# Optimization experiments

Hardware: AMD Instinct MI355X
Metric: run time of the kernel (lower is better)

The kernel has to match this reference:

```python
import jax, jax.numpy as jnp
import numpy as np

B, D, U, R, H, ND = 32768, 1024, 1024, 4, 16, 11


def setup_inputs() -> dict:
    key = jax.random.key(0)
    ks = jax.random.split(key, 12)
    s = 0.02
    return {
        "x": jax.random.normal(ks[0], (B, D), dtype=jnp.float32),
        "domain_indicator": jax.random.randint(ks[1], (B, 1), 0, ND, dtype=jnp.int32),
        "kernel": jax.random.normal(ks[2], (D, U), dtype=jnp.float32) * s,
        "bias": jnp.zeros((U,), dtype=jnp.float32),
        "a_kernel": jax.random.normal(ks[3], (ND, D, R), dtype=jnp.float32) * s,
        "b_kernel": jax.random.normal(ks[4], (ND, R, U), dtype=jnp.float32) * s,
        "domain_bias": jnp.zeros((ND, U), dtype=jnp.float32),
        "WQ": jax.random.normal(ks[5], (R, H), dtype=jnp.float32) * s,
        "WK": jax.random.normal(ks[6], (R, H), dtype=jnp.float32) * s,
        "WV": jax.random.normal(ks[7], (R, H), dtype=jnp.float32) * s,
        "linear": jax.random.normal(ks[8], (H, R), dtype=jnp.float32) * s,
        "factor": jax.random.normal(ks[9], (1, ND), dtype=jnp.float32) * s,
    }


def reference(x, domain_indicator, kernel, bias, a_kernel, b_kernel,
              domain_bias, WQ, WK, WV, linear, factor):
    # Base dense path (dropout inactive at inference)
    out = x @ kernel + bias  # [B, U]

    # Per-domain LoRA-A gather (domains 1..10) and projection: [B, 10, R]
    dA = jnp.einsum('bd,ndr->bnr', x, a_kernel[1:11])

    # Tiny self-attention over the 10 domain projections
    Q = dA @ WQ  # [B, 10, H]
    Kt = dA @ WK
    V = dA @ WV
    scale = 1.0 / jnp.sqrt(jnp.float32(H))
    A = jax.nn.softmax(jnp.einsum('bnh,bmh->bnm', Q, Kt) * scale, axis=-1)
    O = jnp.einsum('bnm,bmh->bnh', A, V) @ linear  # [B, 10, R]

    # Sum over domains -> shared LoRA latent [B, R]
    dom = jnp.sum(O, axis=1)

    # Per-domain LoRA-B expansion: [B, 10, U]
    dB = jnp.einsum('br,nru->bnu', dom, b_kernel[1:11])

    # Domain mixture weights (softmax over all n_domain, cols 1..10 used)
    w = jax.nn.softmax(factor, axis=-1)[0, 1:11]  # [10]
    dout = jnp.einsum('bnu,n->bu', dB, w)  # [B, U]

    # Domain bias from the indicator of the first row
    idx = domain_indicator[0, 0]
    dout = dout + domain_bias[idx]

    return jax.nn.relu(out + dout)
```

## Files before the change

kernel.cpp:

```cpp
#include <hip/hip_runtime.h>
#include <hip/hip_bf16.h>


typedef float f32x4 __attribute__((ext_vector_type(4)));
typedef short s16x8 __attribute__((ext_vector_type(8)));
typedef unsigned int u32x4 __attribute__((ext_vector_type(4)));

#define WS_DOM    0u
#define WS_BEFF   524288u
#define WS_BIAS   540672u
#define WS_G      544768u
#define WS_M      545024u
#define WS_ACATT  545280u
#define WS_KB     679936u
#define WS_XB     2777088u

__device__ __forceinline__ unsigned short f2bf(float f) {
  unsigned int u = __builtin_bit_cast(unsigned int, f);
  u += 0x7fffu + ((u >> 16) & 1u);
  return (unsigned short)(u >> 16);
}
__device__ __forceinline__ unsigned int f2bf2(float a, float b) {
  return (unsigned int)f2bf(a) | ((unsigned int)f2bf(b) << 16);
}

__device__ __forceinline__ void gload_lds16(const void* g, void* l) {
  __builtin_amdgcn_global_load_lds((const __attribute__((address_space(1))) void*)g,
                                   (__attribute__((address_space(3))) void*)l, 16, 0, 0);
}

__global__ void prep1(const float* __restrict__ factor, const float* __restrict__ WQ,
                      const float* __restrict__ WK, const float* __restrict__ WV,
                      const float* __restrict__ linear, const float* __restrict__ bias,
                      const float* __restrict__ domain_bias, const float* __restrict__ b_kernel,
                      const int* __restrict__ dom_ind, float* __restrict__ ws_f) {
  __shared__ float wsm[10];
  const int t = threadIdx.x;
  float* G    = ws_f + (WS_G >> 2);
  float* M    = ws_f + (WS_M >> 2);
  float* beff = ws_f + (WS_BEFF >> 2);
  float* btot = ws_f + (WS_BIAS >> 2);
  if (t == 0) {
    float f[11], mx = -1e30f;
    for (int i = 0; i < 11; i++) { f[i] = factor[i]; mx = fmaxf(mx, f[i]); }
    float s = 0.f;
    for (int i = 0; i < 11; i++) { f[i] = expf(f[i] - mx); s += f[i]; }
    float inv = 1.0f / s;
    for (int i = 0; i < 10; i++) wsm[i] = f[i + 1] * inv;
  }
  if (t < 16) {
    int r = t >> 2, c = t & 3;
    float g = 0.f, m = 0.f;
    for (int h = 0; h < 16; h++) {
      g += WQ[r * 16 + h] * WK[c * 16 + h];
      m += WV[r * 16 + h] * linear[h * 4 + c];
    }
    G[t] = 0.25f * g;
    M[t] = m;
  }
  __syncthreads();
  const int idx = dom_ind[0];
  for (int u = t; u < 1024; u += 256) btot[u] = bias[u] + domain_bias[idx * 1024 + u];
  for (int i = t; i < 4096; i += 256) {
    int r = i >> 10, u = i & 1023;
    float s = 0.f;
    for (int n = 0; n < 10; n++) s += wsm[n] * b_kernel[(1 + n) * 4096 + r * 1024 + u];
    beff[i] = s;
  }
}

__global__ void prep2(const float* __restrict__ a_kernel, unsigned short* __restrict__ acatt) {
  const int i = blockIdx.x * 256 + threadIdx.x;
  const int c = i >> 10, d = i & 1023;
  float v = 0.0f;
  if (c < 40) v = a_kernel[(1 + (c >> 2)) * 4096 + d * 4 + (c & 3)];
  acatt[i] = f2bf(v);
}

__global__ void transK(const float* __restrict__ kern, unsigned short* __restrict__ kb) {
  __shared__ float tile[32][33];
  const int t = threadIdx.x;
  const int kt = blockIdx.x >> 5, nt = blockIdx.x & 31;
  const int k0 = kt << 5, n0 = nt << 5;
  const int row = t >> 5, col = t & 31;
#pragma unroll
  for (int i = 0; i < 4; i++)
    tile[row + i * 8][col] = kern[(k0 + row + i * 8) * 1024 + n0 + col];
  __syncthreads();
  const int nrow = t >> 3, kq = t & 7;
  uint2 pv;
  pv.x = f2bf2(tile[kq * 4 + 0][nrow], tile[kq * 4 + 1][nrow]);
  pv.y = f2bf2(tile[kq * 4 + 2][nrow], tile[kq * 4 + 3][nrow]);
  *reinterpret_cast<uint2*>(&kb[(n0 + nrow) * 1024 + k0 + kq * 4]) = pv;
}

template <bool WRITEXB>
__launch_bounds__(256, 3)
__global__ void stageA(const float* __restrict__ x, const unsigned short* __restrict__ acatt,
                       const float* __restrict__ ws_f, float* __restrict__ dom,
                       unsigned short* __restrict__ xb) {
  __shared__ unsigned short As[16 * 1024];
  __shared__ float dAs[4][16][49];
  const int t = threadIdx.x;
  const int rows0 = blockIdx.x << 4;

  f32x4 v[16];
#pragma unroll
  for (int j = 0; j < 16; j++)
    v[j] = *reinterpret_cast<const f32x4*>(x + (size_t)(rows0 + j) * 1024 + (t << 2));
#pragma unroll
  for (int j = 0; j < 16; j++) {
    uint2 p;
    p.x = f2bf2(v[j][0], v[j][1]);
    p.y = f2bf2(v[j][2], v[j][3]);
    if (WRITEXB)
      *reinterpret_cast<uint2*>(xb + (size_t)(rows0 + j) * 1024 + (t << 2)) = p;
    *reinterpret_cast<uint2*>(As + (((j << 10) + (t << 2)) ^ ((j & 7) << 3))) = p;
  }
  __syncthreads();

  const int w = t >> 6, l = t & 63;
  const int lr = l & 15, kg = l >> 4;
  const f32x4 zero4 = {0.f, 0.f, 0.f, 0.f};
  f32x4 acc[3]; acc[0] = zero4; acc[1] = zero4; acc[2] = zero4;
#pragma unroll
  for (int s = 0; s < 8; s++) {
    const int kelem = (w << 8) + (s << 5) + (kg << 3);
    s16x8 av = *reinterpret_cast<const s16x8*>(As + (((lr << 10) + kelem) ^ ((lr & 7) << 3)));
#pragma unroll
    for (int nf = 0; nf < 3; nf++) {
      s16x8 bv = *reinterpret_cast<const s16x8*>(acatt + ((nf << 4) + lr) * 1024 + kelem);
      acc[nf] = __builtin_amdgcn_mfma_f32_16x16x32_bf16(av, bv, acc[nf], 0, 0, 0);
    }
  }
#pragma unroll
  for (int nf = 0; nf < 3; nf++) {
    const int col = (nf << 4) + lr;
    if (col < 40) {
#pragma unroll
      for (int j = 0; j < 4; j++)
        dAs[w][(kg << 2) + j][col] = acc[nf][j];
    }
  }
  __syncthreads();

  if (t < 16) {
    const int row = t;
    const float* Gp = ws_f + (WS_G >> 2);
    const float* Mp = ws_f + (WS_M >> 2);
    float dA[10][4];
#pragma unroll
    for (int m = 0; m < 10; m++)
#pragma unroll
      for (int r = 0; r < 4; r++)
        dA[m][r] = dAs[0][row][(m << 2) + r] + dAs[1][row][(m << 2) + r]
                 + dAs[2][row][(m << 2) + r] + dAs[3][row][(m << 2) + r];
    float Gv[16], Mv[16];
#pragma unroll
    for (int i = 0; i < 16; i++) { Gv[i] = Gp[i]; Mv[i] = Mp[i]; }
    float tm[10][4];
#pragma unroll
    for (int m = 0; m < 10; m++)
#pragma unroll
      for (int r = 0; r < 4; r++)
        tm[m][r] = Gv[(r << 2) + 0] * dA[m][0] + Gv[(r << 2) + 1] * dA[m][1]
                 + Gv[(r << 2) + 2] * dA[m][2] + Gv[(r << 2) + 3] * dA[m][3];
    float cm[10];
#pragma unroll
    for (int m = 0; m < 10; m++) cm[m] = 0.f;
#pragma unroll
    for (int n = 0; n < 10; n++) {
      float sv[10]; float mx = -1e30f;
#pragma unroll
      for (int m = 0; m < 10; m++) {
        float s = dA[n][0] * tm[m][0] + dA[n][1] * tm[m][1]
                + dA[n][2] * tm[m][2] + dA[n][3] * tm[m][3];
        sv[m] = s; mx = fmaxf(mx, s);
      }
      float ssum = 0.f;
#pragma unroll
      for (int m = 0; m < 10; m++) { float e = expf(sv[m] - mx); sv[m] = e; ssum += e; }
      float inv = 1.0f / ssum;
#pragma unroll
      for (int m = 0; m < 10; m++) cm[m] += sv[m] * inv;
    }
    float u0 = 0.f, u1 = 0.f, u2 = 0.f, u3 = 0.f;
#pragma unroll
    for (int m = 0; m < 10; m++) {
      u0 += cm[m] * dA[m][0]; u1 += cm[m] * dA[m][1];
      u2 += cm[m] * dA[m][2]; u3 += cm[m] * dA[m][3];
    }
    f32x4 dv;
#pragma unroll
    for (int rp = 0; rp < 4; rp++)
      dv[rp] = u0 * Mv[rp] + u1 * Mv[4 + rp] + u2 * Mv[8 + rp] + u3 * Mv[12 + rp];
    *reinterpret_cast<f32x4*>(&dom[(rows0 + row) << 2]) = dv;
  }
}

template <bool XB>
__launch_bounds__(256, 3)
__global__ void mainGEMM(const float* __restrict__ x, const unsigned short* __restrict__ xb,
                         const unsigned short* __restrict__ kb,
                         const float* __restrict__ ws_f, float* __restrict__ out) {
  __shared__ unsigned short As[8192];
  __shared__ unsigned short Bs[8192];
  const int t = threadIdx.x;
  const int w = t >> 6, l = t & 63;
  const int b = blockIdx.x;
  const int xcd = b & 7, i6 = b >> 3;
  const int bm = (xcd << 5) + (i6 >> 3), bn = i6 & 7;
  const int rows0 = bm << 7, cols0 = bn << 7;
  const int wr = w >> 1, wc = w & 1;
  const int lr = l & 15, kg = l >> 4;
  const float* dom  = ws_f + (WS_DOM >> 2);
  const float* beff = ws_f + (WS_BEFF >> 2);
  const float* btot = ws_f + (WS_BIAS >> 2);
  const f32x4 zero4 = {0.f, 0.f, 0.f, 0.f};
  f32x4 acc[4][4];
#pragma unroll
  for (int i = 0; i < 4; i++)
#pragma unroll
    for (int j = 0; j < 4; j++) acc[i][j] = zero4;

#pragma unroll 1
  for (int kc = 0; kc < 16; kc++) {
    if (kc) __syncthreads();
#pragma unroll
    for (int i = 0; i < 4; i++) {
      int segid = i * 256 + t;
      int c = segid >> 3, ks = segid & 7;
      gload_lds16(kb + (cols0 + c) * 1024 + (kc << 6) + ((ks ^ (c & 7)) << 3), Bs + segid * 8);
    }
#pragma unroll
    for (int i = 0; i < 4; i++) {
      int segid = i * 256 + t;
      int row = segid >> 3, ks = segid & 7;
      if (XB) {
        gload_lds16(xb + (rows0 + row) * 1024 + (kc << 6) + ((ks ^ (row & 7)) << 3),
                    As + segid * 8);
      } else {
        const float* gp = x + (rows0 + row) * 1024 + (kc << 6) + (ks << 3);
        f32x4 v0 = *reinterpret_cast<const f32x4*>(gp);
        f32x4 v1 = *reinterpret_cast<const f32x4*>(gp + 4);
        u32x4 o = { f2bf2(v0[0], v0[1]), f2bf2(v0[2], v0[3]),
                    f2bf2(v1[0], v1[1]), f2bf2(v1[2], v1[3]) };
        *reinterpret_cast<u32x4*>(As + row * 64 + ((ks ^ (row & 7)) << 3)) = o;
      }
    }
    __syncthreads();
#pragma unroll
    for (int kh = 0; kh < 2; kh++) {
      const int cp = (kh << 2) + kg;
      s16x8 av[4], bv[4];
#pragma unroll
      for (int mf = 0; mf < 4; mf++) {
        int arow = (wr << 6) + (mf << 4) + lr;
        av[mf] = *reinterpret_cast<const s16x8*>(As + arow * 64 + ((cp ^ (arow & 7)) << 3));
      }
#pragma unroll
      for (int nf = 0; nf < 4; nf++) {
        int brow = (wc << 6) + (nf << 4) + lr;
        bv[nf] = *reinterpret_cast<const s16x8*>(Bs + brow * 64 + ((cp ^ (brow & 7)) << 3));
      }
#pragma unroll
      for (int mf = 0; mf < 4; mf++)
#pragma unroll
        for (int nf = 0; nf < 4; nf++)
          acc[mf][nf] = __builtin_amdgcn_mfma_f32_16x16x32_bf16(av[mf], bv[nf], acc[mf][nf], 0, 0, 0);
    }
  }

  float bcv[4], bev[4][4];
#pragma unroll
  for (int nf = 0; nf < 4; nf++) {
    int col = cols0 + (wc << 6) + (nf << 4) + lr;
    bcv[nf] = btot[col];
#pragma unroll
    for (int r = 0; r < 4; r++) bev[nf][r] = beff[r * 1024 + col];
  }
#pragma unroll
  for (int mf = 0; mf < 4; mf++) {
    const int rbase = rows0 + (wr << 6) + (mf << 4) + (kg << 2);
    f32x4 dm[4];
#pragma unroll
    for (int j = 0; j < 4; j++)
      dm[j] = *reinterpret_cast<const f32x4*>(dom + ((rbase + j) << 2));
#pragma unroll
    for (int nf = 0; nf < 4; nf++) {
      const int col = cols0 + (wc << 6) + (nf << 4) + lr;
#pragma unroll
      for (int j = 0; j < 4; j++) {
        float v = acc[mf][nf][j] + bcv[nf]
                + dm[j][0] * bev[nf][0] + dm[j][1] * bev[nf][1]
                + dm[j][2] * bev[nf][2] + dm[j][3] * bev[nf][3];
        out[(rbase + j) * 1024 + col] = fmaxf(v, 0.f);
      }
    }
  }
}

extern "C" void kernel_launch(void* const* d_in, const int* in_sizes, int n_in,
                              void* d_out, int out_size, void* d_ws, size_t ws_size,
                              hipStream_t stream) {
  (void)in_sizes; (void)n_in; (void)out_size;
  const float* x           = (const float*)d_in[0];
  const int*   dom_ind     = (const int*)d_in[1];
  const float* kern        = (const float*)d_in[2];
  const float* bias        = (const float*)d_in[3];
  const float* a_kernel    = (const float*)d_in[4];
  const float* b_kernel    = (const float*)d_in[5];
  const float* domain_bias = (const float*)d_in[6];
  const float* WQ          = (const float*)d_in[7];
  const float* WK          = (const float*)d_in[8];
  const float* WV          = (const float*)d_in[9];
  const float* linear      = (const float*)d_in[10];
  const float* factor      = (const float*)d_in[11];
  float* out = (float*)d_out;
  char* ws = (char*)d_ws;
  float* ws_f = (float*)ws;
  unsigned short* acatt = (unsigned short*)(ws + WS_ACATT);
  unsigned short* kb    = (unsigned short*)(ws + WS_KB);
  unsigned short* xb    = (unsigned short*)(ws + WS_XB);
  float* dom            = (float*)(ws + WS_DOM);
  const bool use_xb = ws_size >= (size_t)WS_XB + (size_t)32768 * 1024 * 2;

  prep1<<<1, 256, 0, stream>>>(factor, WQ, WK, WV, linear, bias, domain_bias, b_kernel, dom_ind, ws_f);
  prep2<<<256, 256, 0, stream>>>(a_kernel, acatt);
  transK<<<1024, 256, 0, stream>>>(kern, kb);
  if (use_xb) {
    stageA<true><<<2048, 256, 0, stream>>>(x, acatt, ws_f, dom, xb);
    mainGEMM<true><<<2048, 256, 0, stream>>>(x, xb, kb, ws_f, out);
  } else {
    stageA<false><<<2048, 256, 0, stream>>>(x, acatt, ws_f, dom, xb);
    mainGEMM<false><<<2048, 256, 0, stream>>>(x, xb, kb, ws_f, out);
  }
}
```

Measured before the change: 181.3 us.

## Split fp32-to-bf16 conversion of x into separate kernel before LoRA stage

Moves the x fp32-to-bf16 conversion into a dedicated streaming kernel, convX. The LoRA-A stage then reads the bf16 copy into LDS through direct global-to-LDS loads, with a swizzle applied on the global address, and preloads the acatt B fragments into registers before the barrier. This is meant to separate the bandwidth-bound conversion from the MFMA stage and overlap loads. The cost is an extra kernel launch and an extra read of the bf16 x buffer (64 MB) by stageL.

```diff
diff --git a/kernel.cpp b/kernel.cpp
--- a/kernel.cpp
+++ b/kernel.cpp
@@ -94,16 +94,131 @@
   *reinterpret_cast<uint2*>(&kb[(n0 + nrow) * 1024 + k0 + kq * 4]) = pv;
 }
 
-template <bool WRITEXB>
+__global__ void convX(const float* __restrict__ x, unsigned short* __restrict__ xb) {
+  const size_t i0 = (size_t)blockIdx.x * 256 + threadIdx.x;
+#pragma unroll
+  for (int it = 0; it < 8; ++it) {
+    const size_t u = i0 + (size_t)it * 524288;
+    const float* gp = x + u * 8;
+    f32x4 a = *reinterpret_cast<const f32x4*>(gp);
+    f32x4 b = *reinterpret_cast<const f32x4*>(gp + 4);
+    u32x4 o = { f2bf2(a[0], a[1]), f2bf2(a[2], a[3]),
+                f2bf2(b[0], b[1]), f2bf2(b[2], b[3]) };
+    *reinterpret_cast<u32x4*>(xb + u * 8) = o;
+  }
+}
+
 __launch_bounds__(256, 3)
-__global__ void stageA(const float* __restrict__ x, const unsigned short* __restrict__ acatt,
-                       const float* __restrict__ ws_f, float* __restrict__ dom,
-                       unsigned short* __restrict__ xb) {
+__global__ void stageL(const unsigned short* __restrict__ xb,
+                       const unsigned short* __restrict__ acatt,
+                       const float* __restrict__ ws_f, float* __restrict__ dom) {
   __shared__ unsigned short As[16 * 1024];
   __shared__ float dAs[4][16][49];
   const int t = threadIdx.x;
   const int rows0 = blockIdx.x << 4;
-
+  const int w = t >> 6, l = t & 63;
+  const int lr = l & 15, kg = l >> 4;
+
+#pragma unroll
+  for (int i = 0; i < 8; i++) {
+    const int segid = i * 256 + t;
+    const int row = segid >> 7;
+    const int ks = segid & 127;
+    gload_lds16(xb + (size_t)(rows0 + row) * 1024 + ((ks ^ (row & 7)) << 3),
+                As + segid * 8);
+  }
+  s16x8 bvr[8][3];
+#pragma unroll
+  for (int s = 0; s < 8; s++) {
+    const int kelem = (w << 8) + (s << 5) + (kg << 3);
+#pragma unroll
+    for (int nf = 0; nf < 3; nf++)
+      bvr[s][nf] = *reinterpret_cast<const s16x8*>(acatt + ((nf << 4) + lr) * 1024 + kelem);
+  }
+  __syncthreads();
+
+  const f32x4 zero4 = {0.f, 0.f, 0.f, 0.f};
+  f32x4 acc[3]; acc[0] = zero4; acc[1] = zero4; acc[2] = zero4;
+#pragma unroll
+  for (int s = 0; s < 8; s++) {
+    const int kelem = (w << 8) + (s << 5) + (kg << 3);
+    s16x8 av = *reinterpret_cast<const s16x8*>(As + (((lr << 10) + kelem) ^ ((lr & 7) << 3)));
+#pragma unroll
+    for (int nf = 0; nf < 3; nf++)
+      acc[nf] = __builtin_amdgcn_mfma_f32_16x16x32_bf16(av, bvr[s][nf], acc[nf], 0, 0, 0);
+  }
+#pragma unroll
+  for (int nf = 0; nf < 3; nf++) {
+    const int col = (nf << 4) + lr;
+    if (col < 40) {
+#pragma unroll
+      for (int j = 0; j < 4; j++)
+        dAs[w][(kg << 2) + j][col] = acc[nf][j];
+    }
+  }
+  __syncthreads();
+
+  if (t < 16) {
+    const int row = t;
+    const float* Gp = ws_f + (WS_G >> 2);
+    const float* Mp = ws_f + (WS_M >> 2);
+    float dA[10][4];
+#pragma unroll
+    for (int m = 0; m < 10; m++)
+#pragma unroll
+      for (int r = 0; r < 4; r++)
+        dA[m][r] = dAs[0][row][(m << 2) + r] + dAs[1][row][(m << 2) + r]
+                 + dAs[2][row][(m << 2) + r] + dAs[3][row][(m << 2) + r];
+    float Gv[16], Mv[16];
+#pragma unroll
+    for (int i = 0; i < 16; i++) { Gv[i] = Gp[i]; Mv[i] = Mp[i]; }
+    float tm[10][4];
+#pragma unroll
+    for (int m = 0; m < 10; m++)
+#pragma unroll
+      for (int r = 0; r < 4; r++)
+        tm[m][r] = Gv[(r << 2) + 0] * dA[m][0] + Gv[(r << 2) + 1] * dA[m][1]
+                 + Gv[(r << 2) + 2] * dA[m][2] + Gv[(r << 2) + 3] * dA[m][3];
+    float cm[10];
+#pragma unroll
+    for (int m = 0; m < 10; m++) cm[m] = 0.f;
+#pragma unroll
+    for (int n = 0; n < 10; n++) {
+      float sv[10]; float mx = -1e30f;
+#pragma unroll
+      for (int m = 0; m < 10; m++) {
+        float s = dA[n][0] * tm[m][0] + dA[n][1] * tm[m][1]
+                + dA[n][2] * tm[m][2] + dA[n][3] * tm[m][3];
+        sv[m] = s; mx = fmaxf(mx, s);
+      }
+      float ssum = 0.f;
+#pragma unroll
+      for (int m = 0; m < 10; m++) { float e = expf(sv[m] - mx); sv[m] = e; ssum += e; }
+      float inv = 1.0f / ssum;
+#pragma unroll
+      for (int m = 0; m < 10; m++) cm[m] += sv[m] * inv;
+    }
+    float u0 = 0.f, u1 = 0.f, u2 = 0.f, u3 = 0.f;
+#pragma unroll
+    for (int m = 0; m < 10; m++) {
+      u0 += cm[m] * dA[m][0]; u1 += cm[m] * dA[m][1];
+      u2 += cm[m] * dA[m][2]; u3 += cm[m] * dA[m][3];
+    }
+    f32x4 dv;
+#pragma unroll
+    for (int rp = 0; rp < 4; rp++)
+      dv[rp] = u0 * Mv[rp] + u1 * Mv[4 + rp] + u2 * Mv[8 + rp] + u3 * Mv[12 + rp];
+    *reinterpret_cast<f32x4*>(&dom[(rows0 + row) << 2]) = dv;
+  }
+}
+
+__launch_bounds__(256, 3)
+__global__ void stageA_f32(const float* __restrict__ x, const unsigned short* __restrict__ acatt,
+                           const float* __restrict__ ws_f, float* __restrict__ dom) {
+  __shared__ unsigned short As[16 * 1024];
+  __shared__ float dAs[4][16][49];
+  const int t = threadIdx.x;
+  const int rows0 = blockIdx.x << 4;
   f32x4 v[16];
 #pragma unroll
   for (int j = 0; j < 16; j++)
@@ -113,12 +228,9 @@
     uint2 p;
     p.x = f2bf2(v[j][0], v[j][1]);
     p.y = f2bf2(v[j][2], v[j][3]);
-    if (WRITEXB)
-      *reinterpret_cast<uint2*>(xb + (size_t)(rows0 + j) * 1024 + (t << 2)) = p;
     *reinterpret_cast<uint2*>(As + (((j << 10) + (t << 2)) ^ ((j & 7) << 3))) = p;
   }
   __syncthreads();
-
   const int w = t >> 6, l = t & 63;
   const int lr = l & 15, kg = l >> 4;
   const f32x4 zero4 = {0.f, 0.f, 0.f, 0.f};
@@ -143,7 +255,6 @@
     }
   }
   __syncthreads();
-
   if (t < 16) {
     const int row = t;
     const float* Gp = ws_f + (WS_G >> 2);
@@ -329,10 +440,11 @@
   prep2<<<256, 256, 0, stream>>>(a_kernel, acatt);
   transK<<<1024, 256, 0, stream>>>(kern, kb);
   if (use_xb) {
-    stageA<true><<<2048, 256, 0, stream>>>(x, acatt, ws_f, dom, xb);
+    convX<<<2048, 256, 0, stream>>>(x, xb);
+    stageL<<<2048, 256, 0, stream>>>(xb, acatt, ws_f, dom);
     mainGEMM<true><<<2048, 256, 0, stream>>>(x, xb, kb, ws_f, out);
   } else {
-    stageA<false><<<2048, 256, 0, stream>>>(x, acatt, ws_f, dom, xb);
+    stageA_f32<<<2048, 256, 0, stream>>>(x, acatt, ws_f, dom);
     mainGEMM<false><<<2048, 256, 0, stream>>>(x, xb, kb, ws_f, out);
   }
 }
```

Result: slower. 198.1 us (+9.3%).

## Feed LoRA-A MFMA directly from global x, drop LDS staging

Applied to the files above, without the earlier changes.

The LoRA-A projection kernel no longer stages a 16-row bf16 tile of x in shared memory. Each lane now loads its own MFMA A-operand fragment straight from global x, converts it to bf16 in registers, and optionally writes the bf16 copy for the main GEMM. Blocks now cover 32 rows, with waves split into 2 row tiles by 2 K halves, which halves the grid and raises launch bounds to 4 blocks per SM. This removes the 32KB LDS buffer and a barrier to improve occupancy, at the cost of less coalesced global reads: each lane reads 32 contiguous bytes strided by rows.

```diff
diff --git a/kernel.cpp b/kernel.cpp
--- a/kernel.cpp
+++ b/kernel.cpp
@@ -95,41 +95,36 @@
 }
 
 template <bool WRITEXB>
-__launch_bounds__(256, 3)
-__global__ void stageA(const float* __restrict__ x, const unsigned short* __restrict__ acatt,
+__launch_bounds__(256, 4)
+__global__ void stageF(const float* __restrict__ x, const unsigned short* __restrict__ acatt,
                        const float* __restrict__ ws_f, float* __restrict__ dom,
                        unsigned short* __restrict__ xb) {
-  __shared__ unsigned short As[16 * 1024];
-  __shared__ float dAs[4][16][49];
+  __shared__ float dAs[2][2][16][41];
   const int t = threadIdx.x;
-  const int rows0 = blockIdx.x << 4;
-
-  f32x4 v[16];
-#pragma unroll
-  for (int j = 0; j < 16; j++)
-    v[j] = *reinterpret_cast<const f32x4*>(x + (size_t)(rows0 + j) * 1024 + (t << 2));
-#pragma unroll
-  for (int j = 0; j < 16; j++) {
-    uint2 p;
-    p.x = f2bf2(v[j][0], v[j][1]);
-    p.y = f2bf2(v[j][2], v[j][3]);
-    if (WRITEXB)
-      *reinterpret_cast<uint2*>(xb + (size_t)(rows0 + j) * 1024 + (t << 2)) = p;
-    *reinterpret_cast<uint2*>(As + (((j << 10) + (t << 2)) ^ ((j & 7) << 3))) = p;
-  }
-  __syncthreads();
-
   const int w = t >> 6, l = t & 63;
+  const int rt = w >> 1, kh = w & 1;
   const int lr = l & 15, kg = l >> 4;
+  const int rows0 = blockIdx.x << 5;
+  const int grow = rows0 + (rt << 4) + lr;
+  const size_t xrow = (size_t)grow * 1024;
+  const int kbase = (kh << 9) + (kg << 3);
+
   const f32x4 zero4 = {0.f, 0.f, 0.f, 0.f};
   f32x4 acc[3]; acc[0] = zero4; acc[1] = zero4; acc[2] = zero4;
-#pragma unroll
-  for (int s = 0; s < 8; s++) {
-    const int kelem = (w << 8) + (s << 5) + (kg << 3);
-    s16x8 av = *reinterpret_cast<const s16x8*>(As + (((lr << 10) + kelem) ^ ((lr & 7) << 3)));
+
+#pragma unroll 2
+  for (int s = 0; s < 16; s++) {
+    const int k0 = kbase + (s << 5);
+    f32x4 a0 = *reinterpret_cast<const f32x4*>(x + xrow + k0);
+    f32x4 a1 = *reinterpret_cast<const f32x4*>(x + xrow + k0 + 4);
+    u32x4 o = { f2bf2(a0[0], a0[1]), f2bf2(a0[2], a0[3]),
+                f2bf2(a1[0], a1[1]), f2bf2(a1[2], a1[3]) };
+    if (WRITEXB)
+      *reinterpret_cast<u32x4*>(xb + xrow + k0) = o;
+    s16x8 av = __builtin_bit_cast(s16x8, o);
 #pragma unroll
     for (int nf = 0; nf < 3; nf++) {
-      s16x8 bv = *reinterpret_cast<const s16x8*>(acatt + ((nf << 4) + lr) * 1024 + kelem);
+      s16x8 bv = *reinterpret_cast<const s16x8*>(acatt + ((nf << 4) + lr) * 1024 + k0);
       acc[nf] = __builtin_amdgcn_mfma_f32_16x16x32_bf16(av, bv, acc[nf], 0, 0, 0);
     }
   }
@@ -139,13 +134,13 @@
     if (col < 40) {
 #pragma unroll
       for (int j = 0; j < 4; j++)
-        dAs[w][(kg << 2) + j][col] = acc[nf][j];
+        dAs[kh][rt][(kg << 2) + j][col] = acc[nf][j];
     }
   }
   __syncthreads();
 
-  if (t < 16) {
-    const int row = t;
+  if (kh == 0 && l < 16) {
+    const int row = l;
     const float* Gp = ws_f + (WS_G >> 2);
     const float* Mp = ws_f + (WS_M >> 2);
     float dA[10][4];
@@ -153,8 +148,7 @@
     for (int m = 0; m < 10; m++)
 #pragma unroll
       for (int r = 0; r < 4; r++)
-        dA[m][r] = dAs[0][row][(m << 2) + r] + dAs[1][row][(m << 2) + r]
-                 + dAs[2][row][(m << 2) + r] + dAs[3][row][(m << 2) + r];
+        dA[m][r] = dAs[0][rt][row][(m << 2) + r] + dAs[1][rt][row][(m << 2) + r];
     float Gv[16], Mv[16];
 #pragma unroll
     for (int i = 0; i < 16; i++) { Gv[i] = Gp[i]; Mv[i] = Mp[i]; }
@@ -194,7 +188,7 @@
 #pragma unroll
     for (int rp = 0; rp < 4; rp++)
       dv[rp] = u0 * Mv[rp] + u1 * Mv[4 + rp] + u2 * Mv[8 + rp] + u3 * Mv[12 + rp];
-    *reinterpret_cast<f32x4*>(&dom[(rows0 + row) << 2]) = dv;
+    *reinterpret_cast<f32x4*>(&dom[(rows0 + (rt << 4) + row) << 2]) = dv;
   }
 }
 
@@ -329,10 +323,10 @@
   prep2<<<256, 256, 0, stream>>>(a_kernel, acatt);
   transK<<<1024, 256, 0, stream>>>(kern, kb);
   if (use_xb) {
-    stageA<true><<<2048, 256, 0, stream>>>(x, acatt, ws_f, dom, xb);
+    stageF<true><<<1024, 256, 0, stream>>>(x, acatt, ws_f, dom, xb);
     mainGEMM<true><<<2048, 256, 0, stream>>>(x, xb, kb, ws_f, out);
   } else {
-    stageA<false><<<2048, 256, 0, stream>>>(x, acatt, ws_f, dom, xb);
+    stageF<false><<<1024, 256, 0, stream>>>(x, acatt, ws_f, dom, xb);
     mainGEMM<false><<<2048, 256, 0, stream>>>(x, xb, kb, ws_f, out);
   }
 }
```

New measurement: 169.0 us. -6.8%, faster.

## Fuse LoRA-A projection and domain attention into main GEMM kernel

Applied to the files above, without the earlier changes.

Removes the separate stageA kernel and the bf16 copy of x. The main GEMM now reads fp32 x directly, converts it to bf16 in LDS, and computes the 40-column LoRA-A projection as extra MFMAs on the same A tile. After the K loop, each block runs the per-row domain attention in LDS and uses the result in its epilogue. This drops a full pass over x and the xb write/read, but each row's attention is recomputed by all 8 column blocks, and fp32 x reads plus the extra MFMAs add work to the GEMM loop.

```diff
diff --git a/kernel.cpp b/kernel.cpp
--- a/kernel.cpp
+++ b/kernel.cpp
@@ -6,14 +6,12 @@
 typedef short s16x8 __attribute__((ext_vector_type(8)));
 typedef unsigned int u32x4 __attribute__((ext_vector_type(4)));
 
-#define WS_DOM    0u
 #define WS_BEFF   524288u
 #define WS_BIAS   540672u
 #define WS_G      544768u
 #define WS_M      545024u
 #define WS_ACATT  545280u
 #define WS_KB     679936u
-#define WS_XB     2777088u
 
 __device__ __forceinline__ unsigned short f2bf(float f) {
   unsigned int u = __builtin_bit_cast(unsigned int, f);
@@ -94,117 +92,13 @@
   *reinterpret_cast<uint2*>(&kb[(n0 + nrow) * 1024 + k0 + kq * 4]) = pv;
 }
 
-template <bool WRITEXB>
 __launch_bounds__(256, 3)
-__global__ void stageA(const float* __restrict__ x, const unsigned short* __restrict__ acatt,
-                       const float* __restrict__ ws_f, float* __restrict__ dom,
-                       unsigned short* __restrict__ xb) {
-  __shared__ unsigned short As[16 * 1024];
-  __shared__ float dAs[4][16][49];
-  const int t = threadIdx.x;
-  const int rows0 = blockIdx.x << 4;
-
-  f32x4 v[16];
-#pragma unroll
-  for (int j = 0; j < 16; j++)
-    v[j] = *reinterpret_cast<const f32x4*>(x + (size_t)(rows0 + j) * 1024 + (t << 2));
-#pragma unroll
-  for (int j = 0; j < 16; j++) {
-    uint2 p;
-    p.x = f2bf2(v[j][0], v[j][1]);
-    p.y = f2bf2(v[j][2], v[j][3]);
-    if (WRITEXB)
-      *reinterpret_cast<uint2*>(xb + (size_t)(rows0 + j) * 1024 + (t << 2)) = p;
-    *reinterpret_cast<uint2*>(As + (((j << 10) + (t << 2)) ^ ((j & 7) << 3))) = p;
-  }
-  __syncthreads();
-
-  const int w = t >> 6, l = t & 63;
-  const int lr = l & 15, kg = l >> 4;
-  const f32x4 zero4 = {0.f, 0.f, 0.f, 0.f};
-  f32x4 acc[3]; acc[0] = zero4; acc[1] = zero4; acc[2] = zero4;
-#pragma unroll
-  for (int s = 0; s < 8; s++) {
-    const int kelem = (w << 8) + (s << 5) + (kg << 3);
-    s16x8 av = *reinterpret_cast<const s16x8*>(As + (((lr << 10) + kelem) ^ ((lr & 7) << 3)));
-#pragma unroll
-    for (int nf = 0; nf < 3; nf++) {
-      s16x8 bv = *reinterpret_cast<const s16x8*>(acatt + ((nf << 4) + lr) * 1024 + kelem);
-      acc[nf] = __builtin_amdgcn_mfma_f32_16x16x32_bf16(av, bv, acc[nf], 0, 0, 0);
-    }
-  }
-#pragma unroll
-  for (int nf = 0; nf < 3; nf++) {
-    const int col = (nf << 4) + lr;
-    if (col < 40) {
-#pragma unroll
-      for (int j = 0; j < 4; j++)
-        dAs[w][(kg << 2) + j][col] = acc[nf][j];
-    }
-  }
-  __syncthreads();
-
-  if (t < 16) {
-    const int row = t;
-    const float* Gp = ws_f + (WS_G >> 2);
-    const float* Mp = ws_f + (WS_M >> 2);
-    float dA[10][4];
-#pragma unroll
-    for (int m = 0; m < 10; m++)
-#pragma unroll
-      for (int r = 0; r < 4; r++)
-        dA[m][r] = dAs[0][row][(m << 2) + r] + dAs[1][row][(m << 2) + r]
-                 + dAs[2][row][(m << 2) + r] + dAs[3][row][(m << 2) + r];
-    float Gv[16], Mv[16];
-#pragma unroll
-    for (int i = 0; i < 16; i++) { Gv[i] = Gp[i]; Mv[i] = Mp[i]; }
-    float tm[10][4];
-#pragma unroll
-    for (int m = 0; m < 10; m++)
-#pragma unroll
-      for (int r = 0; r < 4; r++)
-        tm[m][r] = Gv[(r << 2) + 0] * dA[m][0] + Gv[(r << 2) + 1] * dA[m][1]
-                 + Gv[(r << 2) + 2] * dA[m][2] + Gv[(r << 2) + 3] * dA[m][3];
-    float cm[10];
-#pragma unroll
-    for (int m = 0; m < 10; m++) cm[m] = 0.f;
-#pragma unroll
-    for (int n = 0; n < 10; n++) {
-      float sv[10]; float mx = -1e30f;
-#pragma unroll
-      for (int m = 0; m < 10; m++) {
-        float s = dA[n][0] * tm[m][0] + dA[n][1] * tm[m][1]
-                + dA[n][2] * tm[m][2] + dA[n][3] * tm[m][3];
-        sv[m] = s; mx = fmaxf(mx, s);
-      }
-      float ssum = 0.f;
-#pragma unroll
-      for (int m = 0; m < 10; m++) { float e = expf(sv[m] - mx); sv[m] = e; ssum += e; }
-      float inv = 1.0f / ssum;
-#pragma unroll
-      for (int m = 0; m < 10; m++) cm[m] += sv[m] * inv;
-    }
-    float u0 = 0.f, u1 = 0.f, u2 = 0.f, u3 = 0.f;
-#pragma unroll
-    for (int m = 0; m < 10; m++) {
-      u0 += cm[m] * dA[m][0]; u1 += cm[m] * dA[m][1];
-      u2 += cm[m] * dA[m][2]; u3 += cm[m] * dA[m][3];
-    }
-    f32x4 dv;
-#pragma unroll
-    for (int rp = 0; rp < 4; rp++)
-      dv[rp] = u0 * Mv[rp] + u1 * Mv[4 + rp] + u2 * Mv[8 + rp] + u3 * Mv[12 + rp];
-    *reinterpret_cast<f32x4*>(&dom[(rows0 + row) << 2]) = dv;
-  }
-}
-
-template <bool XB>
-__launch_bounds__(256, 3)
-__global__ void mainGEMM(const float* __restrict__ x, const unsigned short* __restrict__ xb,
-                         const unsigned short* __restrict__ kb,
-                         const float* __restrict__ ws_f, float* __restrict__ out) {
-  __shared__ unsigned short As[8192];
-  __shared__ unsigned short Bs[8192];
+__global__ void fusedGEMM(const float* __restrict__ x, const unsigned short* __restrict__ kb,
+                          const unsigned short* __restrict__ acatt,
+                          const float* __restrict__ ws_f, float* __restrict__ out) {
+  __shared__ __align__(16) char smem[32768];
+  unsigned short* As = (unsigned short*)smem;
+  unsigned short* Bs = (unsigned short*)(smem + 16384);
   const int t = threadIdx.x;
   const int w = t >> 6, l = t & 63;
   const int b = blockIdx.x;
@@ -213,7 +107,6 @@
   const int rows0 = bm << 7, cols0 = bn << 7;
   const int wr = w >> 1, wc = w & 1;
   const int lr = l & 15, kg = l >> 4;
-  const float* dom  = ws_f + (WS_DOM >> 2);
   const float* beff = ws_f + (WS_BEFF >> 2);
   const float* btot = ws_f + (WS_BIAS >> 2);
   const f32x4 zero4 = {0.f, 0.f, 0.f, 0.f};
@@ -222,6 +115,11 @@
   for (int i = 0; i < 4; i++)
 #pragma unroll
     for (int j = 0; j < 4; j++) acc[i][j] = zero4;
+  f32x4 accd[2][3];
+#pragma unroll
+  for (int i = 0; i < 2; i++)
+#pragma unroll
+    for (int j = 0; j < 3; j++) accd[i][j] = zero4;
 
 #pragma unroll 1
   for (int kc = 0; kc < 16; kc++) {
@@ -236,18 +134,20 @@
     for (int i = 0; i < 4; i++) {
       int segid = i * 256 + t;
       int row = segid >> 3, ks = segid & 7;
-      if (XB) {
-        gload_lds16(xb + (rows0 + row) * 1024 + (kc << 6) + ((ks ^ (row & 7)) << 3),
-                    As + segid * 8);
-      } else {
-        const float* gp = x + (rows0 + row) * 1024 + (kc << 6) + (ks << 3);
-        f32x4 v0 = *reinterpret_cast<const f32x4*>(gp);
-        f32x4 v1 = *reinterpret_cast<const f32x4*>(gp + 4);
-        u32x4 o = { f2bf2(v0[0], v0[1]), f2bf2(v0[2], v0[3]),
-                    f2bf2(v1[0], v1[1]), f2bf2(v1[2], v1[3]) };
-        *reinterpret_cast<u32x4*>(As + row * 64 + ((ks ^ (row & 7)) << 3)) = o;
-      }
-    }
+      const float* gp = x + (size_t)(rows0 + row) * 1024 + (kc << 6) + (ks << 3);
+      f32x4 v0 = *reinterpret_cast<const f32x4*>(gp);
+      f32x4 v1 = *reinterpret_cast<const f32x4*>(gp + 4);
+      u32x4 o = { f2bf2(v0[0], v0[1]), f2bf2(v0[2], v0[3]),
+                  f2bf2(v1[0], v1[1]), f2bf2(v1[2], v1[3]) };
+      *reinterpret_cast<u32x4*>(As + row * 64 + ((ks ^ (row & 7)) << 3)) = o;
+    }
+    s16x8 bd[2][3];
+#pragma unroll
+    for (int kh = 0; kh < 2; kh++)
+#pragma unroll
+      for (int nf = 0; nf < 3; nf++)
+        bd[kh][nf] = *reinterpret_cast<const s16x8*>(
+            acatt + ((nf << 4) + lr) * 1024 + (kc << 6) + (kh << 5) + (kg << 3));
     __syncthreads();
 #pragma unroll
     for (int kh = 0; kh < 2; kh++) {
@@ -268,8 +168,82 @@
 #pragma unroll
         for (int nf = 0; nf < 4; nf++)
           acc[mf][nf] = __builtin_amdgcn_mfma_f32_16x16x32_bf16(av[mf], bv[nf], acc[mf][nf], 0, 0, 0);
-    }
-  }
+#pragma unroll
+      for (int mf2 = 0; mf2 < 2; mf2++) {
+        int arow2 = (w << 5) + (mf2 << 4) + lr;
+        s16x8 av2 = *reinterpret_cast<const s16x8*>(As + arow2 * 64 + ((cp ^ (arow2 & 7)) << 3));
+#pragma unroll
+        for (int nf = 0; nf < 3; nf++)
+          accd[mf2][nf] = __builtin_amdgcn_mfma_f32_16x16x32_bf16(av2, bd[kh][nf], accd[mf2][nf], 0, 0, 0);
+      }
+    }
+  }
+
+  __syncthreads();
+  float (*dAs)[41] = (float(*)[41])smem;
+  float (*domL)[4] = (float(*)[4])(smem + 20992);
+#pragma unroll
+  for (int mf2 = 0; mf2 < 2; mf2++)
+#pragma unroll
+    for (int nf = 0; nf < 3; nf++) {
+      const int col = (nf << 4) + lr;
+      if (col < 40) {
+#pragma unroll
+        for (int j = 0; j < 4; j++)
+          dAs[(w << 5) + (mf2 << 4) + (kg << 2) + j][col] = accd[mf2][nf][j];
+      }
+    }
+  __syncthreads();
+  if (t < 128) {
+    const int row = t;
+    const float* Gp = ws_f + (WS_G >> 2);
+    const float* Mp = ws_f + (WS_M >> 2);
+    float Gv[16];
+#pragma unroll
+    for (int i = 0; i < 16; i++) Gv[i] = Gp[i];
+    float tm[10][4];
+#pragma unroll
+    for (int m = 0; m < 10; m++) {
+      float d0 = dAs[row][(m << 2) + 0], d1 = dAs[row][(m << 2) + 1];
+      float d2 = dAs[row][(m << 2) + 2], d3 = dAs[row][(m << 2) + 3];
+#pragma unroll
+      for (int r = 0; r < 4; r++)
+        tm[m][r] = Gv[(r << 2) + 0] * d0 + Gv[(r << 2) + 1] * d1
+                 + Gv[(r << 2) + 2] * d2 + Gv[(r << 2) + 3] * d3;
+    }
+    float cm[10];
+#pragma unroll
+    for (int m = 0; m < 10; m++) cm[m] = 0.f;
+#pragma unroll
+    for (int n = 0; n < 10; n++) {
+      float d0 = dAs[row][(n << 2) + 0], d1 = dAs[row][(n << 2) + 1];
+      float d2 = dAs[row][(n << 2) + 2], d3 = dAs[row][(n << 2) + 3];
+      float sv[10]; float mx = -1e30f;
+#pragma unroll
+      for (int m = 0; m < 10; m++) {
+        float s = d0 * tm[m][0] + d1 * tm[m][1] + d2 * tm[m][2] + d3 * tm[m][3];
+        sv[m] = s; mx = fmaxf(mx, s);
+      }
+      float ssum = 0.f;
+#pragma unroll
+      for (int m = 0; m < 10; m++) { float e = expf(sv[m] - mx); sv[m] = e; ssum += e; }
+      float inv = 1.0f / ssum;
+#pragma unroll
+      for (int m = 0; m < 10; m++) cm[m] += sv[m] * inv;
+    }
+    float u0 = 0.f, u1 = 0.f, u2 = 0.f, u3 = 0.f;
+#pragma unroll
+    for (int m = 0; m < 10; m++) {
+      u0 += cm[m] * dAs[row][(m << 2) + 0];
+      u1 += cm[m] * dAs[row][(m << 2) + 1];
+      u2 += cm[m] * dAs[row][(m << 2) + 2];
+      u3 += cm[m] * dAs[row][(m << 2) + 3];
+    }
+#pragma unroll
+    for (int rp = 0; rp < 4; rp++)
+      domL[row][rp] = u0 * Mp[rp] + u1 * Mp[4 + rp] + u2 * Mp[8 + rp] + u3 * Mp[12 + rp];
+  }
+  __syncthreads();
 
   float bcv[4], bev[4][4];
 #pragma unroll
@@ -281,11 +255,11 @@
   }
 #pragma unroll
   for (int mf = 0; mf < 4; mf++) {
-    const int rbase = rows0 + (wr << 6) + (mf << 4) + (kg << 2);
+    const int lbase = (wr << 6) + (mf << 4) + (kg << 2);
     f32x4 dm[4];
 #pragma unroll
     for (int j = 0; j < 4; j++)
-      dm[j] = *reinterpret_cast<const f32x4*>(dom + ((rbase + j) << 2));
+      dm[j] = *reinterpret_cast<const f32x4*>(domL[lbase + j]);
 #pragma unroll
     for (int nf = 0; nf < 4; nf++) {
       const int col = cols0 + (wc << 6) + (nf << 4) + lr;
@@ -294,7 +268,7 @@
         float v = acc[mf][nf][j] + bcv[nf]
                 + dm[j][0] * bev[nf][0] + dm[j][1] * bev[nf][1]
                 + dm[j][2] * bev[nf][2] + dm[j][3] * bev[nf][3];
-        out[(rbase + j) * 1024 + col] = fmaxf(v, 0.f);
+        out[(size_t)(rows0 + lbase + j) * 1024 + col] = fmaxf(v, 0.f);
       }
     }
   }
@@ -303,7 +277,7 @@
 extern "C" void kernel_launch(void* const* d_in, const int* in_sizes, int n_in,
                               void* d_out, int out_size, void* d_ws, size_t ws_size,
                               hipStream_t stream) {
-  (void)in_sizes; (void)n_in; (void)out_size;
+  (void)in_sizes; (void)n_in; (void)out_size; (void)ws_size;
   const float* x           = (const float*)d_in[0];
   const int*   dom_ind     = (const int*)d_in[1];
   const float* kern        = (const float*)d_in[2];
@@ -321,18 +295,9 @@
   float* ws_f = (float*)ws;
   unsigned short* acatt = (unsigned short*)(ws + WS_ACATT);
   unsigned short* kb    = (unsigned short*)(ws + WS_KB);
-  unsigned short* xb    = (unsigned short*)(ws + WS_XB);
-  float* dom            = (float*)(ws + WS_DOM);
-  const bool use_xb = ws_size >= (size_t)WS_XB + (size_t)32768 * 1024 * 2;
 
   prep1<<<1, 256, 0, stream>>>(factor, WQ, WK, WV, linear, bias, domain_bias, b_kernel, dom_ind, ws_f);
   prep2<<<256, 256, 0, stream>>>(a_kernel, acatt);
   transK<<<1024, 256, 0, stream>>>(kern, kb);
-  if (use_xb) {
-    stageA<true><<<2048, 256, 0, stream>>>(x, acatt, ws_f, dom, xb);
-    mainGEMM<true><<<2048, 256, 0, stream>>>(x, xb, kb, ws_f, out);
-  } else {
-    stageA<false><<<2048, 256, 0, stream>>>(x, acatt, ws_f, dom, xb);
-    mainGEMM<false><<<2048, 256, 0, stream>>>(x, xb, kb, ws_f, out);
-  }
-}
+  fusedGEMM<<<2048, 256, 0, stream>>>(x, kb, acatt, ws_f, out);
+}
```

Result: slower. 292.2 us (+61.1%).
